# Kernel tuning notes

Hardware: AMD Instinct MI355X
Metric: run time of the kernel (lower is better)

The kernel has to match this reference:

```python
import jax, jax.numpy as jnp
import numpy as np

N_FEATURES = 512
N_LAYERS = 128
BATCH = 2048
PI = np.pi


def setup_inputs() -> dict:
    key = jax.random.key(0)
    k0, k1, k2, k3, k4 = jax.random.split(key, 5)
    nA = N_FEATURES // 2            # angles per A layer (even pairs)
    nB = (N_FEATURES - 1) // 2      # angles per B layer (odd pairs)
    LB = N_LAYERS // 2
    LA = N_LAYERS - LB              # equal when N_LAYERS even
    return {
        "cmplx": jax.random.normal(k0, (BATCH, N_FEATURES, 2), dtype=jnp.float32),
        "angleA0": jax.random.uniform(k1, (LA, nA), jnp.float32, -PI, PI),
        "angleA1": jax.random.uniform(k2, (LA, nA), jnp.float32, -PI, PI),
        "angleB0": jax.random.uniform(k3, (LB, nB), jnp.float32, -PI, PI),
        "angleB1": jax.random.uniform(k4, (LB, nB), jnp.float32, -PI, PI),
        "omega": jnp.zeros((N_FEATURES,), jnp.float32),
    }


def _mzi(a, b, ang0, ang1):
    # MZI = DC . PS(ang1) . DC . PS(ang0) acting on mode pair (a, b)
    # U = 1/2 [[e^{i phi}(e^{i th}-1),    i(e^{i th}+1)   ],
    #          [i e^{i phi}(e^{i th}+1),  (1 - e^{i th})  ]]
    ephi = jnp.exp(1j * ang0)
    eth = jnp.exp(1j * ang1)
    t = 0.5 * (eth - 1.0)
    u = 0.5 * (eth + 1.0)
    na = ephi * t * a + 1j * u * b
    nb = 1j * ephi * u * a - t * b
    return na, nb


def _layer_A(x, a0, a1):
    # pairs (0,1),(2,3),...
    a = x[:, 0::2]
    b = x[:, 1::2]
    na, nb = _mzi(a, b, a0, a1)
    return jnp.stack([na, nb], axis=-1).reshape(x.shape)


def _layer_B(x, b0, b1):
    # pairs (1,2),(3,4),...; endpoints 0 and N-1 pass through (N even)
    N = x.shape[1]
    a = x[:, 1:N - 1:2]
    b = x[:, 2:N:2]
    na, nb = _mzi(a, b, b0, b1)
    mid = jnp.stack([na, nb], axis=-1).reshape(x.shape[0], N - 2)
    return jnp.concatenate([x[:, :1], mid, x[:, -1:]], axis=1)


def reference(cmplx, angleA0, angleA1, angleB0, angleB1, omega):
    x = cmplx[..., 0] + 1j * cmplx[..., 1]   # [B, N] complex64

    def step(x, angs):
        a0, a1, b0, b1 = angs
        x = _layer_A(x, a0, a1)
        x = _layer_B(x, b0, b1)
        return x, None

    x, _ = jax.lax.scan(step, x, (angleA0, angleA1, angleB0, angleB1))
    out = x * jnp.exp(1j * omega)            # complex diagonal phase
    return jnp.stack([out.real, out.imag], axis=-1)
```

## Files before the change

### kernel.cpp

```cpp
#include <hip/hip_runtime.h>

#define NF 512
#define MB 2048
#define CSTRIDE 256
#define PL (NF * NF)
#define LDT 72

typedef __attribute__((ext_vector_type(8))) short bf16x8;
typedef __attribute__((ext_vector_type(4))) float f32x4;
typedef __attribute__((ext_vector_type(4))) int i32x4;

__device__ __forceinline__ float2 cmul(float2 a, float2 b) {
  return make_float2(fmaf(a.x, b.x, -(a.y * b.y)), fmaf(a.x, b.y, a.y * b.x));
}
__device__ __forceinline__ float2 cfma(float2 a, float2 b, float2 c) {
  return make_float2(fmaf(a.x, b.x, fmaf(-a.y, b.y, c.x)),
                     fmaf(a.x, b.y, fmaf(a.y, b.x, c.y)));
}
__device__ __forceinline__ unsigned short f2bf(float f) {
  union { float f; unsigned u; } v; v.f = f;
  unsigned r = v.u + 0x7FFF + ((v.u >> 16) & 1);
  return (unsigned short)(r >> 16);
}

__global__ __launch_bounds__(256) void prep_kernel(
    const float* __restrict__ a0, const float* __restrict__ a1,
    const float* __restrict__ b0, const float* __restrict__ b1,
    float4* __restrict__ cA, float4* __restrict__ cB)
{
  const int l = blockIdx.x, tid = threadIdx.x;
  {
    float ang0 = a0[l * 256 + tid], ang1 = a1[l * 256 + tid];
    float se, ce, st, ct;
    sincosf(ang0, &se, &ce);
    sincosf(ang1, &st, &ct);
    float2 ephi = make_float2(ce, se);
    float2 tt = make_float2(0.5f * (ct - 1.0f), 0.5f * st);
    float2 uu = make_float2(0.5f * (ct + 1.0f), 0.5f * st);
    float2 C1 = cmul(ephi, tt);
    float2 C2 = make_float2(-uu.y, uu.x);
    float2 eu = cmul(ephi, uu);
    float2 C3 = make_float2(-eu.y, eu.x);
    float2 C4 = make_float2(-tt.x, -tt.y);
    float4* dst = cA + (size_t)(l * CSTRIDE + tid) * 2;
    dst[0] = make_float4(C1.x, C1.y, C2.x, C2.y);
    dst[1] = make_float4(C3.x, C3.y, C4.x, C4.y);
  }
  if (tid < 255) {
    float ang0 = b0[l * 255 + tid], ang1 = b1[l * 255 + tid];
    float se, ce, st, ct;
    sincosf(ang0, &se, &ce);
    sincosf(ang1, &st, &ct);
    float2 ephi = make_float2(ce, se);
    float2 tt = make_float2(0.5f * (ct - 1.0f), 0.5f * st);
    float2 uu = make_float2(0.5f * (ct + 1.0f), 0.5f * st);
    float2 C1 = cmul(ephi, tt);
    float2 C2 = make_float2(-uu.y, uu.x);
    float2 eu = cmul(ephi, uu);
    float2 C3 = make_float2(-eu.y, eu.x);
    float2 C4 = make_float2(-tt.x, -tt.y);
    float4* dst = cB + (size_t)(l * CSTRIDE + tid) * 2;
    dst[0] = make_float4(C1.x, C1.y, C2.x, C2.y);
    dst[1] = make_float4(C3.x, C3.y, C4.x, C4.y);
  } else {
    float4* dst = cB + (size_t)(l * CSTRIDE + 255) * 2;
    dst[0] = make_float4(0.f, 0.f, 0.f, 0.f);
    dst[1] = make_float4(0.f, 0.f, 0.f, 0.f);
  }
}

struct MZS { float2 a0, b0, a1, b1; };

__device__ __forceinline__ void mzi_apply(const float4& k0, const float4& k1,
                                          float2& a, float2& b) {
  float2 c1 = make_float2(k0.x, k0.y), c2 = make_float2(k0.z, k0.w);
  float2 c3 = make_float2(k1.x, k1.y), c4 = make_float2(k1.z, k1.w);
  float2 na = cfma(c2, b, cmul(c1, a));
  float2 nb = cfma(c4, b, cmul(c3, a));
  a = na; b = nb;
}
__device__ __forceinline__ float2 mzi_bnd(const float4& k0, const float4& k1,
                                          float2& a, float2 b, bool en) {
  float2 d1 = make_float2(k0.x, k0.y), d2 = make_float2(k0.z, k0.w);
  float2 d3 = make_float2(k1.x, k1.y), d4 = make_float2(k1.z, k1.w);
  float2 na = cfma(d2, b, cmul(d1, a));
  float2 nb = cfma(d4, b, cmul(d3, a));
  if (en) a = na;
  return en ? nb : make_float2(0.f, 0.f);
}
__device__ __forceinline__ void load_bank(float4 (&K)[8],
    const float4* __restrict__ cA, const float4* __restrict__ cB, int l, int q0)
{
  const float4* pa = cA + (size_t)l * (CSTRIDE * 2) + (size_t)q0 * 2;
  const float4* pb = cB + (size_t)l * (CSTRIDE * 2) + (size_t)q0 * 2;
  K[0] = pa[0]; K[1] = pa[1]; K[2] = pa[2]; K[3] = pa[3];
  K[4] = pb[0]; K[5] = pb[1]; K[6] = pb[2]; K[7] = pb[3];
}
__device__ __forceinline__ void step_state(const float4 (&K)[8], int L, bool hasBnd,
                                           MZS& s)
{
  mzi_apply(K[0], K[1], s.a0, s.b0);
  mzi_apply(K[2], K[3], s.a1, s.b1);
  float xnx = __shfl_down(s.a0.x, 1);
  float xny = __shfl_down(s.a0.y, 1);
  float2 xn = (L == 63) ? make_float2(0.f, 0.f) : make_float2(xnx, xny);
  float2 nbo = mzi_bnd(K[6], K[7], s.b1, xn, hasBnd);
  mzi_apply(K[4], K[5], s.b0, s.a1);
  float px = __shfl_up(nbo.x, 1);
  float py = __shfl_up(nbo.y, 1);
  if (L > 0) s.a0 = make_float2(px, py);
}

__global__ __launch_bounds__(64) void chunk_mesh(
    const float4* __restrict__ cA, const float4* __restrict__ cB,
    unsigned short* __restrict__ Cb)
{
  const int bid = blockIdx.x;
  const int m = bid >> 9;
  const int cb = bid & 511;
  const int j = (cb & 7) * 64 + (cb >> 3);
  const int L = threadIdx.x;
  const int p0 = j >> 1;
  int ws = p0 - 63; ws = ws < 0 ? 0 : (ws > 128 ? 128 : ws);
  const int q0 = ws + 2 * L, q1 = q0 + 1;
  const bool hasBnd = (q1 < 255);

  MZS s;
  s.a0 = make_float2((2 * q0     == j) ? 1.f : 0.f, 0.f);
  s.b0 = make_float2((2 * q0 + 1 == j) ? 1.f : 0.f, 0.f);
  s.a1 = make_float2((2 * q1     == j) ? 1.f : 0.f, 0.f);
  s.b1 = make_float2((2 * q1 + 1 == j) ? 1.f : 0.f, 0.f);

  const int l0 = m * 32;
  float4 K0[8], K1[8], K2[8];
  load_bank(K0, cA, cB, l0 + 0, q0);
  load_bank(K1, cA, cB, l0 + 1, q0);
  load_bank(K2, cA, cB, l0 + 2, q0);

#pragma unroll 1
  for (int i = 0; i < 30; i += 3) {
    step_state(K0, L, hasBnd, s);
    load_bank(K0, cA, cB, l0 + ((i + 3 < 32) ? i + 3 : 31), q0);
    step_state(K1, L, hasBnd, s);
    load_bank(K1, cA, cB, l0 + ((i + 4 < 32) ? i + 4 : 31), q0);
    step_state(K2, L, hasBnd, s);
    load_bank(K2, cA, cB, l0 + ((i + 5 < 32) ? i + 5 : 31), q0);
  }
  step_state(K0, L, hasBnd, s);
  step_state(K1, L, hasBnd, s);

  unsigned short* Cr = Cb + (size_t)m * 2 * PL;
  unsigned short* Ci = Cr + PL;
  const int rows[4] = {2 * q0, 2 * q0 + 1, 2 * q1, 2 * q1 + 1};
  const float2 vals[4] = {s.a0, s.b0, s.a1, s.b1};
#pragma unroll
  for (int e = 0; e < 4; ++e) {
    Cr[(size_t)rows[e] * NF + j] = f2bf(vals[e].x);
    Ci[(size_t)rows[e] * NF + j] = f2bf(vals[e].y);
  }
#pragma unroll
  for (int e = 0; e < 4; ++e) {
    const int row = (2 * ws + 256 + 4 * L + e) & 511;
    Cr[(size_t)row * NF + j] = 0;
    Ci[(size_t)row * NF + j] = 0;
  }
}

template <int MODE>
__global__ __launch_bounds__(256) void gemm_kernel(
    const float2* __restrict__ Xf,
    const unsigned short* __restrict__ Zr, const unsigned short* __restrict__ Zi,
    const unsigned short* __restrict__ Cr, const unsigned short* __restrict__ Ci,
    unsigned short* __restrict__ Or, unsigned short* __restrict__ Oi,
    const float* __restrict__ omega, float2* __restrict__ Y)
{
  __shared__ __align__(16) unsigned short Ars[32][LDT];
  __shared__ __align__(16) unsigned short Ais[32][LDT];
  __shared__ __align__(16) unsigned short Brs[64][LDT];
  __shared__ __align__(16) unsigned short Bis[64][LDT];

  const int tid = threadIdx.x;
  const int w = tid >> 6, wm = w & 1, wn = w >> 1;
  const int lane = tid & 63;
  const int bm = (blockIdx.x >> 3) * 32;
  const int bn = (blockIdx.x & 7) * 64;

  int klo = bn - 72; if (klo < 0) klo = 0; klo &= ~63;
  int khi = bn + 136; if (khi > NF) khi = NF; khi = (khi + 63) & ~63;

  f32x4 acc_r[2], acc_i[2];
#pragma unroll
  for (int nf = 0; nf < 2; ++nf) {
    acc_r[nf] = (f32x4){0.f, 0.f, 0.f, 0.f};
    acc_i[nf] = (f32x4){0.f, 0.f, 0.f, 0.f};
  }
  const int sar = tid >> 3, sak = (tid & 7) * 8;
  const int sbr = tid >> 2, sbk = (tid & 3) * 16;

  for (int k0 = klo; k0 < khi; k0 += 64) {
    ushort4 ar2[2], ai2[2];
    if (MODE == 0) {
      const float4* xs = (const float4*)(Xf + (size_t)(bm + sar) * NF + k0 + sak);
#pragma unroll
      for (int h = 0; h < 2; ++h) {
        float4 v0 = xs[2 * h], v1 = xs[2 * h + 1];
        ar2[h].x = f2bf(v0.x); ai2[h].x = f2bf(v0.y);
        ar2[h].y = f2bf(v0.z); ai2[h].y = f2bf(v0.w);
        ar2[h].z = f2bf(v1.x); ai2[h].z = f2bf(v1.y);
        ar2[h].w = f2bf(v1.z); ai2[h].w = f2bf(v1.w);
      }
    } else {
      const ushort4* gr = (const ushort4*)(Zr + (size_t)(bm + sar) * NF + k0 + sak);
      const ushort4* gi = (const ushort4*)(Zi + (size_t)(bm + sar) * NF + k0 + sak);
      ar2[0] = gr[0]; ar2[1] = gr[1];
      ai2[0] = gi[0]; ai2[1] = gi[1];
    }
    const uint4* gbr = (const uint4*)(Cr + (size_t)(bn + sbr) * NF + k0 + sbk);
    const uint4* gbi = (const uint4*)(Ci + (size_t)(bn + sbr) * NF + k0 + sbk);
    uint4 br0 = gbr[0], br1 = gbr[1];
    uint4 bi0 = gbi[0], bi1 = gbi[1];

    if (k0 > klo) __syncthreads();

    *(ushort4*)&Ars[sar][sak]     = ar2[0];
    *(ushort4*)&Ars[sar][sak + 4] = ar2[1];
    *(ushort4*)&Ais[sar][sak]     = ai2[0];
    *(ushort4*)&Ais[sar][sak + 4] = ai2[1];
    *(uint4*)&Brs[sbr][sbk]       = br0;
    *(uint4*)&Brs[sbr][sbk + 8]   = br1;
    *(uint4*)&Bis[sbr][sbk]       = bi0;
    *(uint4*)&Bis[sbr][sbk + 8]   = bi1;

    __syncthreads();

#pragma unroll
    for (int kk = 0; kk < 2; ++kk) {
      const int ko = kk * 32 + (lane >> 4) * 8;
      bf16x8 afr = *(const bf16x8*)&Ars[wm * 16 + (lane & 15)][ko];
      bf16x8 afi = *(const bf16x8*)&Ais[wm * 16 + (lane & 15)][ko];
      i32x4 neg = (i32x4)afi ^ (int)0x80008000;
      bf16x8 afin = (bf16x8)neg;
#pragma unroll
      for (int nf = 0; nf < 2; ++nf) {
        bf16x8 bfr = *(const bf16x8*)&Brs[wn * 32 + nf * 16 + (lane & 15)][ko];
        bf16x8 bfi = *(const bf16x8*)&Bis[wn * 32 + nf * 16 + (lane & 15)][ko];
        acc_r[nf] = __builtin_amdgcn_mfma_f32_16x16x32_bf16(afr,  bfr, acc_r[nf], 0, 0, 0);
        acc_r[nf] = __builtin_amdgcn_mfma_f32_16x16x32_bf16(afin, bfi, acc_r[nf], 0, 0, 0);
        acc_i[nf] = __builtin_amdgcn_mfma_f32_16x16x32_bf16(afr,  bfi, acc_i[nf], 0, 0, 0);
        acc_i[nf] = __builtin_amdgcn_mfma_f32_16x16x32_bf16(afi,  bfr, acc_i[nf], 0, 0, 0);
      }
    }
  }

  const int dn0 = bn + wn * 32 + (lane & 15);
  const int dm0 = bm + wm * 16 + (lane >> 4) * 4;
#pragma unroll
  for (int nf = 0; nf < 2; ++nf) {
    const int n = dn0 + nf * 16;
    if (MODE == 1) {
      float sn, cn;
      sincosf(omega[n], &sn, &cn);
#pragma unroll
      for (int r = 0; r < 4; ++r) {
        float yr = acc_r[nf][r], yi = acc_i[nf][r];
        Y[(size_t)(dm0 + r) * NF + n] =
            make_float2(fmaf(yr, cn, -(yi * sn)), fmaf(yr, sn, yi * cn));
      }
    } else {
#pragma unroll
      for (int r = 0; r < 4; ++r) {
        Or[(size_t)(dm0 + r) * NF + n] = f2bf(acc_r[nf][r]);
        Oi[(size_t)(dm0 + r) * NF + n] = f2bf(acc_i[nf][r]);
      }
    }
  }
}

extern "C" void kernel_launch(void* const* d_in, const int* in_sizes, int n_in,
                              void* d_out, int out_size, void* d_ws, size_t ws_size,
                              hipStream_t stream) {
  const float2* Xf   = (const float2*)d_in[0];
  const float* a0    = (const float*)d_in[1];
  const float* a1    = (const float*)d_in[2];
  const float* b0    = (const float*)d_in[3];
  const float* b1    = (const float*)d_in[4];
  const float* omega = (const float*)d_in[5];

  size_t off = 0;
  float4* cA = (float4*)((char*)d_ws + off); off += (size_t)64 * CSTRIDE * 2 * sizeof(float4);
  float4* cB = (float4*)((char*)d_ws + off); off += (size_t)64 * CSTRIDE * 2 * sizeof(float4);
  unsigned short* Cb  = (unsigned short*)((char*)d_ws + off); off += (size_t)2 * 2 * PL * 2;
  unsigned short* Z1r = (unsigned short*)((char*)d_ws + off); off += (size_t)MB * NF * 2;
  unsigned short* Z1i = (unsigned short*)((char*)d_ws + off); off += (size_t)MB * NF * 2;
  float2* Y = (float2*)d_out;

  const unsigned short* C0r = Cb;           const unsigned short* C0i = Cb + PL;
  const unsigned short* C1r = Cb + 2 * PL;  const unsigned short* C1i = Cb + 3 * PL;

  prep_kernel<<<64, 256, 0, stream>>>(a0, a1, b0, b1, cA, cB);
  chunk_mesh<<<1024, 64, 0, stream>>>(cA, cB, Cb);

  const int grid = (MB / 32) * (NF / 64);
  gemm_kernel<0><<<grid, 256, 0, stream>>>(Xf, nullptr, nullptr, C0r, C0i,
                                           Z1r, Z1i, omega, Y);
  gemm_kernel<1><<<grid, 256, 0, stream>>>(nullptr, Z1r, Z1i, C1r, C1i,
                                           nullptr, nullptr, omega, Y);
}
```

Measured before the change: 49.02 us.

## Compose four 16-layer banded chunk matrices into one unitary before single batch GEMM

The mesh is now split into four 16-layer chunks instead of two 32-layer chunks, which shortens the serial per-thread state stepping. Even chunks are written in transposed layout. Two small banded matrix-product kernels then combine the chunks into a single 512x512 unitary. This replaces two batch GEMMs and the bf16 intermediate activation round-trip with one wider-band batch GEMM. In exchange it adds two kernel launches and extra bf16 rounding in the composed matrix, and the final GEMM must cover a wider band of K.

```diff
diff --git a/kernel.cpp b/kernel.cpp
--- a/kernel.cpp
+++ b/kernel.cpp
@@ -131,47 +131,176 @@
   s.a1 = make_float2((2 * q1     == j) ? 1.f : 0.f, 0.f);
   s.b1 = make_float2((2 * q1 + 1 == j) ? 1.f : 0.f, 0.f);
 
-  const int l0 = m * 32;
-  float4 K0[8], K1[8], K2[8];
+  const int l0 = m * 16;
+  float4 K0[8], K1[8];
   load_bank(K0, cA, cB, l0 + 0, q0);
   load_bank(K1, cA, cB, l0 + 1, q0);
-  load_bank(K2, cA, cB, l0 + 2, q0);
-
 #pragma unroll 1
-  for (int i = 0; i < 30; i += 3) {
+  for (int i = 0; i < 14; i += 2) {
     step_state(K0, L, hasBnd, s);
-    load_bank(K0, cA, cB, l0 + ((i + 3 < 32) ? i + 3 : 31), q0);
+    load_bank(K0, cA, cB, l0 + ((i + 2 < 16) ? i + 2 : 15), q0);
     step_state(K1, L, hasBnd, s);
-    load_bank(K1, cA, cB, l0 + ((i + 4 < 32) ? i + 4 : 31), q0);
-    step_state(K2, L, hasBnd, s);
-    load_bank(K2, cA, cB, l0 + ((i + 5 < 32) ? i + 5 : 31), q0);
+    load_bank(K1, cA, cB, l0 + ((i + 3 < 16) ? i + 3 : 15), q0);
   }
   step_state(K0, L, hasBnd, s);
   step_state(K1, L, hasBnd, s);
 
   unsigned short* Cr = Cb + (size_t)m * 2 * PL;
   unsigned short* Ci = Cr + PL;
-  const int rows[4] = {2 * q0, 2 * q0 + 1, 2 * q1, 2 * q1 + 1};
-  const float2 vals[4] = {s.a0, s.b0, s.a1, s.b1};
-#pragma unroll
-  for (int e = 0; e < 4; ++e) {
-    Cr[(size_t)rows[e] * NF + j] = f2bf(vals[e].x);
-    Ci[(size_t)rows[e] * NF + j] = f2bf(vals[e].y);
-  }
-#pragma unroll
-  for (int e = 0; e < 4; ++e) {
-    const int row = (2 * ws + 256 + 4 * L + e) & 511;
-    Cr[(size_t)row * NF + j] = 0;
-    Ci[(size_t)row * NF + j] = 0;
-  }
-}
-
-template <int MODE>
+  if ((m & 1) == 0) {
+    const int col0 = 2 * q0;
+    ushort4 vr, vi;
+    vr.x = f2bf(s.a0.x); vr.y = f2bf(s.b0.x); vr.z = f2bf(s.a1.x); vr.w = f2bf(s.b1.x);
+    vi.x = f2bf(s.a0.y); vi.y = f2bf(s.b0.y); vi.z = f2bf(s.a1.y); vi.w = f2bf(s.b1.y);
+    *(ushort4*)&Cr[(size_t)j * NF + col0] = vr;
+    *(ushort4*)&Ci[(size_t)j * NF + col0] = vi;
+    const int z0 = (col0 + 256) & 511;
+    const int z1 = (col0 + 258) & 511;
+    const ushort2 zz = make_ushort2(0, 0);
+    *(ushort2*)&Cr[(size_t)j * NF + z0] = zz;
+    *(ushort2*)&Cr[(size_t)j * NF + z1] = zz;
+    *(ushort2*)&Ci[(size_t)j * NF + z0] = zz;
+    *(ushort2*)&Ci[(size_t)j * NF + z1] = zz;
+  } else {
+    const int rows[4] = {2 * q0, 2 * q0 + 1, 2 * q1, 2 * q1 + 1};
+    const float2 vals[4] = {s.a0, s.b0, s.a1, s.b1};
+#pragma unroll
+    for (int e = 0; e < 4; ++e) {
+      Cr[(size_t)rows[e] * NF + j] = f2bf(vals[e].x);
+      Ci[(size_t)rows[e] * NF + j] = f2bf(vals[e].y);
+    }
+#pragma unroll
+    for (int e = 0; e < 4; ++e) {
+      const int row = (2 * ws + 256 + 4 * L + e) & 511;
+      Cr[(size_t)row * NF + j] = 0;
+      Ci[(size_t)row * NF + j] = 0;
+    }
+  }
+}
+
+__device__ void prod_tile(
+    const unsigned short* __restrict__ Agr, const unsigned short* __restrict__ Agi,
+    const unsigned short* __restrict__ Bgr, const unsigned short* __restrict__ Bgi,
+    unsigned short* __restrict__ Or, unsigned short* __restrict__ Oi,
+    int bm, int bn, int klo, int khi, int tid,
+    unsigned short (*Ars)[LDT], unsigned short (*Ais)[LDT],
+    unsigned short (*Brs)[LDT], unsigned short (*Bis)[LDT])
+{
+  const int w = tid >> 6, wm = w & 1, wn = w >> 1, lane = tid & 63;
+  f32x4 acc_r[2], acc_i[2];
+#pragma unroll
+  for (int nf = 0; nf < 2; ++nf) {
+    acc_r[nf] = (f32x4){0.f, 0.f, 0.f, 0.f};
+    acc_i[nf] = (f32x4){0.f, 0.f, 0.f, 0.f};
+  }
+  const int sar = tid >> 3, sak = (tid & 7) * 8;
+  const int sbr = tid >> 2, sbk = (tid & 3) * 16;
+
+  for (int k0 = klo; k0 < khi; k0 += 64) {
+    const uint4* gar = (const uint4*)(Agr + (size_t)(bm + sar) * NF + k0 + sak);
+    const uint4* gai = (const uint4*)(Agi + (size_t)(bm + sar) * NF + k0 + sak);
+    const uint4* gbr = (const uint4*)(Bgr + (size_t)(bn + sbr) * NF + k0 + sbk);
+    const uint4* gbi = (const uint4*)(Bgi + (size_t)(bn + sbr) * NF + k0 + sbk);
+    uint4 ar = gar[0];
+    uint4 ai = gai[0];
+    uint4 br0 = gbr[0], br1 = gbr[1];
+    uint4 bi0 = gbi[0], bi1 = gbi[1];
+
+    __syncthreads();
+
+    *(uint4*)&Ars[sar][sak]     = ar;
+    *(uint4*)&Ais[sar][sak]     = ai;
+    *(uint4*)&Brs[sbr][sbk]     = br0;
+    *(uint4*)&Brs[sbr][sbk + 8] = br1;
+    *(uint4*)&Bis[sbr][sbk]     = bi0;
+    *(uint4*)&Bis[sbr][sbk + 8] = bi1;
+
+    __syncthreads();
+
+#pragma unroll
+    for (int kk = 0; kk < 2; ++kk) {
+      const int ko = kk * 32 + (lane >> 4) * 8;
+      bf16x8 afr = *(const bf16x8*)&Ars[wm * 16 + (lane & 15)][ko];
+      bf16x8 afi = *(const bf16x8*)&Ais[wm * 16 + (lane & 15)][ko];
+      i32x4 neg = (i32x4)afi ^ (int)0x80008000;
+      bf16x8 afin = (bf16x8)neg;
+#pragma unroll
+      for (int nf = 0; nf < 2; ++nf) {
+        bf16x8 bfr = *(const bf16x8*)&Brs[wn * 32 + nf * 16 + (lane & 15)][ko];
+        bf16x8 bfi = *(const bf16x8*)&Bis[wn * 32 + nf * 16 + (lane & 15)][ko];
+        acc_r[nf] = __builtin_amdgcn_mfma_f32_16x16x32_bf16(afr,  bfr, acc_r[nf], 0, 0, 0);
+        acc_r[nf] = __builtin_amdgcn_mfma_f32_16x16x32_bf16(afin, bfi, acc_r[nf], 0, 0, 0);
+        acc_i[nf] = __builtin_amdgcn_mfma_f32_16x16x32_bf16(afr,  bfi, acc_i[nf], 0, 0, 0);
+        acc_i[nf] = __builtin_amdgcn_mfma_f32_16x16x32_bf16(afi,  bfr, acc_i[nf], 0, 0, 0);
+      }
+    }
+  }
+
+  const int dn0 = bn + wn * 32 + (lane & 15);
+  const int dm0 = bm + wm * 16 + (lane >> 4) * 4;
+#pragma unroll
+  for (int nf = 0; nf < 2; ++nf) {
+    const int n = dn0 + nf * 16;
+#pragma unroll
+    for (int r = 0; r < 4; ++r) {
+      Or[(size_t)(dm0 + r) * NF + n] = f2bf(acc_r[nf][r]);
+      Oi[(size_t)(dm0 + r) * NF + n] = f2bf(acc_i[nf][r]);
+    }
+  }
+}
+
+__global__ __launch_bounds__(256) void prodW_kernel(
+    const unsigned short* __restrict__ Cb, unsigned short* __restrict__ Wp)
+{
+  __shared__ __align__(16) unsigned short Ars[32][LDT];
+  __shared__ __align__(16) unsigned short Ais[32][LDT];
+  __shared__ __align__(16) unsigned short Brs[64][LDT];
+  __shared__ __align__(16) unsigned short Bis[64][LDT];
+
+  const int tid = threadIdx.x;
+  const int z = blockIdx.x >> 7;
+  const int t = blockIdx.x & 127;
+  const int bm = (t >> 3) * 32, bn = (t & 7) * 64;
+  const unsigned short* CT = Cb + (size_t)(2 * z) * 2 * PL;
+  const unsigned short* CN = Cb + (size_t)(2 * z + 1) * 2 * PL;
+  unsigned short* O = Wp + (size_t)z * 2 * PL;
+  const int hw = 35;
+  const unsigned short* A; const unsigned short* B;
+  if (z == 0) { A = CT; B = CN; }
+  else        { A = CN; B = CT; }
+  int klo = bm - hw; { int u = bn - hw; if (u > klo) klo = u; }
+  if (klo < 0) klo = 0; klo &= ~63;
+  int khi = bm + 32 + hw; { int u = bn + 64 + hw; if (u < khi) khi = u; }
+  if (khi > NF) khi = NF; khi = (khi + 63) & ~63;
+  prod_tile(A, A + PL, B, B + PL, O, O + PL, bm, bn, klo, khi, tid,
+            Ars, Ais, Brs, Bis);
+}
+
+__global__ __launch_bounds__(256) void prodU_kernel(
+    const unsigned short* __restrict__ Wp, unsigned short* __restrict__ Up)
+{
+  __shared__ __align__(16) unsigned short Ars[32][LDT];
+  __shared__ __align__(16) unsigned short Ais[32][LDT];
+  __shared__ __align__(16) unsigned short Brs[64][LDT];
+  __shared__ __align__(16) unsigned short Bis[64][LDT];
+
+  const int tid = threadIdx.x;
+  const int t = blockIdx.x;
+  const int bm = (t >> 3) * 32, bn = (t & 7) * 64;
+  const unsigned short* W0T = Wp;
+  const unsigned short* W1N = Wp + (size_t)2 * PL;
+  const int hw = 70;
+  int klo = bm - hw; { int u = bn - hw; if (u > klo) klo = u; }
+  if (klo < 0) klo = 0; klo &= ~63;
+  int khi = bm + 32 + hw; { int u = bn + 64 + hw; if (u < khi) khi = u; }
+  if (khi > NF) khi = NF; khi = (khi + 63) & ~63;
+  prod_tile(W1N, W1N + PL, W0T, W0T + PL, Up, Up + PL, bm, bn, klo, khi, tid,
+            Ars, Ais, Brs, Bis);
+}
+
 __global__ __launch_bounds__(256) void gemm_kernel(
     const float2* __restrict__ Xf,
-    const unsigned short* __restrict__ Zr, const unsigned short* __restrict__ Zi,
-    const unsigned short* __restrict__ Cr, const unsigned short* __restrict__ Ci,
-    unsigned short* __restrict__ Or, unsigned short* __restrict__ Oi,
+    const unsigned short* __restrict__ Ur, const unsigned short* __restrict__ Ui,
     const float* __restrict__ omega, float2* __restrict__ Y)
 {
   __shared__ __align__(16) unsigned short Ars[32][LDT];
@@ -185,8 +314,8 @@
   const int bm = (blockIdx.x >> 3) * 32;
   const int bn = (blockIdx.x & 7) * 64;
 
-  int klo = bn - 72; if (klo < 0) klo = 0; klo &= ~63;
-  int khi = bn + 136; if (khi > NF) khi = NF; khi = (khi + 63) & ~63;
+  int klo = bn - 140; if (klo < 0) klo = 0; klo &= ~63;
+  int khi = bn + 204; if (khi > NF) khi = NF; khi = (khi + 63) & ~63;
 
   f32x4 acc_r[2], acc_i[2];
 #pragma unroll
@@ -199,24 +328,17 @@
 
   for (int k0 = klo; k0 < khi; k0 += 64) {
     ushort4 ar2[2], ai2[2];
-    if (MODE == 0) {
-      const float4* xs = (const float4*)(Xf + (size_t)(bm + sar) * NF + k0 + sak);
-#pragma unroll
-      for (int h = 0; h < 2; ++h) {
-        float4 v0 = xs[2 * h], v1 = xs[2 * h + 1];
-        ar2[h].x = f2bf(v0.x); ai2[h].x = f2bf(v0.y);
-        ar2[h].y = f2bf(v0.z); ai2[h].y = f2bf(v0.w);
-        ar2[h].z = f2bf(v1.x); ai2[h].z = f2bf(v1.y);
-        ar2[h].w = f2bf(v1.z); ai2[h].w = f2bf(v1.w);
-      }
-    } else {
-      const ushort4* gr = (const ushort4*)(Zr + (size_t)(bm + sar) * NF + k0 + sak);
-      const ushort4* gi = (const ushort4*)(Zi + (size_t)(bm + sar) * NF + k0 + sak);
-      ar2[0] = gr[0]; ar2[1] = gr[1];
-      ai2[0] = gi[0]; ai2[1] = gi[1];
-    }
-    const uint4* gbr = (const uint4*)(Cr + (size_t)(bn + sbr) * NF + k0 + sbk);
-    const uint4* gbi = (const uint4*)(Ci + (size_t)(bn + sbr) * NF + k0 + sbk);
+    const float4* xs = (const float4*)(Xf + (size_t)(bm + sar) * NF + k0 + sak);
+#pragma unroll
+    for (int h = 0; h < 2; ++h) {
+      float4 v0 = xs[2 * h], v1 = xs[2 * h + 1];
+      ar2[h].x = f2bf(v0.x); ai2[h].x = f2bf(v0.y);
+      ar2[h].y = f2bf(v0.z); ai2[h].y = f2bf(v0.w);
+      ar2[h].z = f2bf(v1.x); ai2[h].z = f2bf(v1.y);
+      ar2[h].w = f2bf(v1.z); ai2[h].w = f2bf(v1.w);
+    }
+    const uint4* gbr = (const uint4*)(Ur + (size_t)(bn + sbr) * NF + k0 + sbk);
+    const uint4* gbi = (const uint4*)(Ui + (size_t)(bn + sbr) * NF + k0 + sbk);
     uint4 br0 = gbr[0], br1 = gbr[1];
     uint4 bi0 = gbi[0], bi1 = gbi[1];
 
@@ -257,21 +379,13 @@
 #pragma unroll
   for (int nf = 0; nf < 2; ++nf) {
     const int n = dn0 + nf * 16;
-    if (MODE == 1) {
-      float sn, cn;
-      sincosf(omega[n], &sn, &cn);
-#pragma unroll
-      for (int r = 0; r < 4; ++r) {
-        float yr = acc_r[nf][r], yi = acc_i[nf][r];
-        Y[(size_t)(dm0 + r) * NF + n] =
-            make_float2(fmaf(yr, cn, -(yi * sn)), fmaf(yr, sn, yi * cn));
-      }
-    } else {
-#pragma unroll
-      for (int r = 0; r < 4; ++r) {
-        Or[(size_t)(dm0 + r) * NF + n] = f2bf(acc_r[nf][r]);
-        Oi[(size_t)(dm0 + r) * NF + n] = f2bf(acc_i[nf][r]);
-      }
+    float sn, cn;
+    sincosf(omega[n], &sn, &cn);
+#pragma unroll
+    for (int r = 0; r < 4; ++r) {
+      float yr = acc_r[nf][r], yi = acc_i[nf][r];
+      Y[(size_t)(dm0 + r) * NF + n] =
+          make_float2(fmaf(yr, cn, -(yi * sn)), fmaf(yr, sn, yi * cn));
     }
   }
 }
@@ -289,20 +403,14 @@
   size_t off = 0;
   float4* cA = (float4*)((char*)d_ws + off); off += (size_t)64 * CSTRIDE * 2 * sizeof(float4);
   float4* cB = (float4*)((char*)d_ws + off); off += (size_t)64 * CSTRIDE * 2 * sizeof(float4);
-  unsigned short* Cb  = (unsigned short*)((char*)d_ws + off); off += (size_t)2 * 2 * PL * 2;
-  unsigned short* Z1r = (unsigned short*)((char*)d_ws + off); off += (size_t)MB * NF * 2;
-  unsigned short* Z1i = (unsigned short*)((char*)d_ws + off); off += (size_t)MB * NF * 2;
+  unsigned short* Cb = (unsigned short*)((char*)d_ws + off); off += (size_t)4 * 2 * PL * 2;
+  unsigned short* Wp = (unsigned short*)((char*)d_ws + off); off += (size_t)2 * 2 * PL * 2;
+  unsigned short* Up = (unsigned short*)((char*)d_ws + off); off += (size_t)1 * 2 * PL * 2;
   float2* Y = (float2*)d_out;
 
-  const unsigned short* C0r = Cb;           const unsigned short* C0i = Cb + PL;
-  const unsigned short* C1r = Cb + 2 * PL;  const unsigned short* C1i = Cb + 3 * PL;
-
   prep_kernel<<<64, 256, 0, stream>>>(a0, a1, b0, b1, cA, cB);
-  chunk_mesh<<<1024, 64, 0, stream>>>(cA, cB, Cb);
-
-  const int grid = (MB / 32) * (NF / 64);
-  gemm_kernel<0><<<grid, 256, 0, stream>>>(Xf, nullptr, nullptr, C0r, C0i,
-                                           Z1r, Z1i, omega, Y);
-  gemm_kernel<1><<<grid, 256, 0, stream>>>(nullptr, Z1r, Z1i, C1r, C1i,
-                                           nullptr, nullptr, omega, Y);
-}
+  chunk_mesh<<<2048, 64, 0, stream>>>(cA, cB, Cb);
+  prodW_kernel<<<256, 256, 0, stream>>>(Cb, Wp);
+  prodU_kernel<<<128, 256, 0, stream>>>(Wp, Up);
+  gemm_kernel<<<(MB / 32) * (NF / 64), 256, 0, stream>>>(Xf, Up, Up + PL, omega, Y);
+}
```

New measurement: 52.62 us. 1.07x slower.
